# Performance work log

Measured on AMD Instinct MI355X. Metric: run time of the kernel, lower is better.

Reference implementation:

```python
import jax, jax.numpy as jnp
import numpy as np

B, S, D, H = 4, 4096, 512, 8


def setup_inputs() -> dict:
    key = jax.random.key(0)
    ks = jax.random.split(key, 9)
    s = 1.0 / np.sqrt(D)
    return {
        "x": jax.random.normal(ks[0], (B, S, D), jnp.float32),
        "Wq": jax.random.normal(ks[1], (D, D), jnp.float32) * s,
        "bq": jax.random.normal(ks[2], (D,), jnp.float32) * 0.02,
        "Wk": jax.random.normal(ks[3], (D, D), jnp.float32) * s,
        "bk": jax.random.normal(ks[4], (D,), jnp.float32) * 0.02,
        "Wv": jax.random.normal(ks[5], (D, D), jnp.float32) * s,
        "bv": jax.random.normal(ks[6], (D,), jnp.float32) * 0.02,
        "Wo": jax.random.normal(ks[7], (H * D, D), jnp.float32) * (1.0 / np.sqrt(H * D)),
        "bo": jax.random.normal(ks[8], (D,), jnp.float32) * 0.02,
        "num_heads": H,
    }


def reference(x, Wq, bq, Wk, bk, Wv, bv, Wo, bo, num_heads):
    # Q/K/V projections (self-attention path; encoder_output=None)
    q = x @ Wq + bq  # [B,S,D]
    k = x @ Wk + bk
    v = x @ Wv + bv
    scale = 1.0 / jnp.sqrt(jnp.asarray(x.shape[-1], x.dtype))
    scores = jnp.einsum("bqd,bkd->bqk", q, k) * scale  # [B,S,S]
    probs = jax.nn.softmax(scores, axis=-1)
    attn = jnp.einsum("bqk,bkd->bqd", probs, v)  # [B,S,D]
    # Original stacks identical heads then torch.cat along dim=-1 -> tile H copies.
    cat = jnp.tile(attn, (1, 1, num_heads))  # [B,S,H*D]
    return cat @ Wo + bo  # [B,S,D]
```

## Files before the change

kernel.cpp:

```cpp
#include <hip/hip_runtime.h>
#include <stdint.h>

#define SCALE 0.04419417382415922f

typedef __bf16 bf16x8 __attribute__((ext_vector_type(8)));
typedef float f32x4 __attribute__((ext_vector_type(4)));
typedef uint16_t u16x8 __attribute__((ext_vector_type(8)));

static __device__ __forceinline__ uint16_t f2bf(float f) {
  union { float f; uint32_t u; } v; v.f = f;
  uint32_t u = v.u;
  return (uint16_t)((u + 0x7FFFu + ((u >> 16) & 1u)) >> 16);
}

static __device__ __forceinline__ void gload16(const void* g, void* l) {
  __builtin_amdgcn_global_load_lds(
      (__attribute__((address_space(1))) void*)g,
      (__attribute__((address_space(3))) void*)l, 16, 0, 0);
}

#define P_BAR asm volatile("s_barrier" ::: "memory")
#define P_LGKM do { asm volatile("s_waitcnt lgkmcnt(0)" ::: "memory"); \
                    __builtin_amdgcn_sched_barrier(0); } while (0)


__global__ __launch_bounds__(256)
void convert_x(const float* __restrict__ x, uint16_t* __restrict__ xb) {
  size_t i = ((size_t)blockIdx.x * 256 + threadIdx.x) * 8;
  float4 a = *(const float4*)(x + i);
  float4 b = *(const float4*)(x + i + 4);
  u16x8 o;
  o[0] = f2bf(a.x); o[1] = f2bf(a.y); o[2] = f2bf(a.z); o[3] = f2bf(a.w);
  o[4] = f2bf(b.x); o[5] = f2bf(b.y); o[6] = f2bf(b.z); o[7] = f2bf(b.w);
  *(u16x8*)(xb + i) = o;
}

__global__ __launch_bounds__(256)
void pack_w(const float* __restrict__ Wq, const float* __restrict__ Wk,
            const float* __restrict__ Wv, uint16_t* __restrict__ wt) {
  __shared__ float tile[64][65];
  const int k0 = blockIdx.x * 64, n0 = blockIdx.y * 64, m = blockIdx.z;
  const float* W = (m == 0) ? Wq : ((m == 1) ? Wk : Wv);
  const float scl = (m == 0) ? SCALE : 1.0f;
  const int t = threadIdx.x, r = t >> 2, c0 = (t & 3) * 16;
  #pragma unroll
  for (int j = 0; j < 4; j++) {
    float4 v = *(const float4*)&W[(size_t)(k0 + r) * 512 + n0 + c0 + j * 4];
    tile[r][c0 + j * 4 + 0] = v.x; tile[r][c0 + j * 4 + 1] = v.y;
    tile[r][c0 + j * 4 + 2] = v.z; tile[r][c0 + j * 4 + 3] = v.w;
  }
  __syncthreads();
  u16x8 o0, o1;
  #pragma unroll
  for (int e = 0; e < 8; e++) {
    o0[e] = f2bf(tile[c0 + e][r] * scl);
    o1[e] = f2bf(tile[c0 + 8 + e][r] * scl);
  }
  uint16_t* dst = wt + (size_t)(m * 512 + n0 + r) * 512 + k0 + c0;
  *(u16x8*)dst = o0;
  *(u16x8*)(dst + 8) = o1;
}

__global__ __launch_bounds__(256)
void pack_wo(const float* __restrict__ Wo, uint16_t* __restrict__ woT) {
  __shared__ float tile[64][65];
  const int k0 = blockIdx.x * 64, n0 = blockIdx.y * 64;
  const int t = threadIdx.x, r = t >> 2, c0 = (t & 3) * 16;
  float av[16];
  #pragma unroll
  for (int e = 0; e < 16; e++) av[e] = 0.f;
  for (int h = 0; h < 8; h++) {
    const float* src = &Wo[(size_t)(h * 512 + k0 + r) * 512 + n0 + c0];
    #pragma unroll
    for (int j = 0; j < 4; j++) {
      float4 v = *(const float4*)(src + j * 4);
      av[j * 4 + 0] += v.x; av[j * 4 + 1] += v.y;
      av[j * 4 + 2] += v.z; av[j * 4 + 3] += v.w;
    }
  }
  #pragma unroll
  for (int e = 0; e < 16; e++) tile[r][c0 + e] = av[e];
  __syncthreads();
  u16x8 o0, o1;
  #pragma unroll
  for (int e = 0; e < 8; e++) {
    o0[e] = f2bf(tile[c0 + e][r]);
    o1[e] = f2bf(tile[c0 + 8 + e][r]);
  }
  uint16_t* dst = woT + (size_t)(n0 + r) * 512 + k0 + c0;
  *(u16x8*)dst = o0;
  *(u16x8*)(dst + 8) = o1;
}

__global__ void pack_bias(const float* __restrict__ bq, const float* __restrict__ bk,
                          const float* __restrict__ bv, float* __restrict__ bqkv) {
  int i = blockIdx.x * 256 + threadIdx.x;
  if (i < 512) bqkv[i] = bq[i] * SCALE;
  else if (i < 1024) bqkv[i] = bk[i - 512];
  else if (i < 1536) bqkv[i] = bv[i - 1024];
}

__global__ __launch_bounds__(256)
void transpose_v(const uint16_t* __restrict__ qkv, uint16_t* __restrict__ Vt) {
  __shared__ uint16_t tile[64][72];
  const int s0 = blockIdx.x * 64, d0 = blockIdx.y * 64, b = blockIdx.z;
  const int t = threadIdx.x, r = t >> 2, c0 = (t & 3) * 16;
  const uint16_t* src = qkv + ((size_t)(b * 4096 + s0 + r)) * 1536 + 1024 + d0 + c0;
  *(u16x8*)&tile[r][c0] = *(const u16x8*)src;
  *(u16x8*)&tile[r][c0 + 8] = *(const u16x8*)(src + 8);
  __syncthreads();
  u16x8 o0, o1;
  #pragma unroll
  for (int e = 0; e < 8; e++) { o0[e] = tile[c0 + e][r]; o1[e] = tile[c0 + 8 + e][r]; }
  uint16_t* dst = Vt + ((size_t)b * 512 + d0 + r) * 4096 + s0 + c0;
  *(u16x8*)dst = o0;
  *(u16x8*)(dst + 8) = o1;
}

template<int BN, int MODE>
__global__ __launch_bounds__(512, 2)
void gemm8(const uint16_t* __restrict__ A, const uint16_t* __restrict__ Bt,
           const float* __restrict__ bias, void* __restrict__ Cout,
           float* __restrict__ sums,
           int M, int N, int K, int lda, int ldb, int ldc,
           long long aZ, long long bZ, long long cZ, long long sZ) {
  constexpr int NREP = BN / 64;
  constexpr int NH = NREP / 2;
  constexpr int WN = BN / 4;
  constexpr int BELTS = BN * 64;
  __shared__ uint16_t SH[32768 + 2 * BELTS];

  const int nbn = N / BN;
  const int nwg = (M >> 8) * nbn;
  int id = blockIdx.x;
  id = (id & 7) * (nwg >> 3) + (id >> 3);
  const int bm = id / nbn, bn = id % nbn;
  const long long z = blockIdx.z;
  A += z * aZ; Bt += z * bZ;
  const size_t m0 = (size_t)bm * 256, n0 = (size_t)bn * BN;

  const int t = threadIdx.x;
  const int lane = t & 63, w = t >> 6;
  const int wr = w >> 2, wc = w & 3;
  const int l15 = lane & 15, l4 = lane >> 4, l7 = lane & 7, l3 = lane >> 3;
  const int sw = l7 ^ l3;

  const uint16_t* srcA = A + (m0 + w * 8 + l3) * (size_t)lda + sw * 8;
  const uint16_t* srcB = (BN == 256)
      ? Bt + (n0 + (w >> 1) * 64 + (w & 1) * 16 + l3) * (size_t)ldb + sw * 8
      : Bt + (n0 + (w >> 1) * 32 + (w & 1) * 8 + l3) * (size_t)ldb + sw * 8;

  const int NKT = K >> 6;
  const int NIT = NKT >> 1;

  f32x4 acc[8][NREP];
  #pragma unroll
  for (int i = 0; i < 8; i++)
    #pragma unroll
    for (int j = 0; j < NREP; j++) acc[i][j] = (f32x4)(0.f);

  bf16x8 a[4][2], b0[NH][2], b1[NH][2];

  auto stageA = [&](int tile, int mh) {
    const uint16_t* s = srcA + mh * 64 * (size_t)lda + tile * 64;
    uint16_t* d = SH + (tile & 1) * 16384 + mh * 4096 + w * 512;
    gload16(s, d);
    gload16(s + 128 * (size_t)lda, d + 8192);
  };
  auto stageB = [&](int tile, int nh) {
    if (BN == 256) {
      const uint16_t* s = srcB + nh * 32 * (size_t)ldb + tile * 64;
      uint16_t* d = SH + 32768 + (tile & 1) * BELTS + (w >> 1) * 4096 + nh * 2048 + (w & 1) * 1024;
      gload16(s, d);
      gload16(s + 8 * (size_t)ldb, d + 512);
    } else {
      const uint16_t* s = srcB + nh * 16 * (size_t)ldb + tile * 64;
      uint16_t* d = SH + 32768 + (tile & 1) * BELTS + (w >> 1) * 2048 + nh * 1024 + (w & 1) * 512;
      gload16(s, d);
    }
  };
  auto loadA = [&](int buf, int mh) {
    const uint16_t* base = SH + buf * 16384 + (wr * 128 + mh * 64 + l15) * 64;
    #pragma unroll
    for (int m = 0; m < 4; m++)
      #pragma unroll
      for (int ks = 0; ks < 2; ks++)
        a[m][ks] = *(const bf16x8*)(base + m * 1024 + (((ks * 4 + l4) ^ l7) * 8));
  };
  auto loadB = [&](int buf, int nh, bf16x8 (&bd)[NH][2]) {
    const uint16_t* base = SH + 32768 + buf * BELTS + (wc * WN + nh * (WN / 2) + l15) * 64;
    #pragma unroll
    for (int n = 0; n < NH; n++)
      #pragma unroll
      for (int ks = 0; ks < 2; ks++)
        bd[n][ks] = *(const bf16x8*)(base + n * 1024 + (((ks * 4 + l4) ^ l7) * 8));
  };
  auto quad = [&](int mh, int nq, bf16x8 (&bq)[NH][2]) {
    __builtin_amdgcn_s_setprio(1);
    #pragma unroll
    for (int m = 0; m < 4; m++)
      #pragma unroll
      for (int n = 0; n < NH; n++)
        #pragma unroll
        for (int ks = 0; ks < 2; ks++)
          acc[mh * 4 + m][nq + n] = __builtin_amdgcn_mfma_f32_16x16x32_bf16(
              a[m][ks], bq[n][ks], acc[mh * 4 + m][nq + n], 0, 0, 0);
    __builtin_amdgcn_s_setprio(0);
  };

  stageA(0, 0); stageB(0, 0); stageA(0, 1); stageB(0, 1);
  stageA(1, 0); stageB(1, 0); stageA(1, 1);
  if (BN == 256) asm volatile("s_waitcnt vmcnt(6)" ::: "memory");
  else           asm volatile("s_waitcnt vmcnt(5)" ::: "memory");
  P_BAR;

  for (int k = 0; k < NIT - 1; ++k) {
    const int tt = 2 * k;
    loadA(0, 0); loadB(0, 0, b0); stageB(tt + 1, 1);
    P_BAR; P_LGKM; quad(0, 0, b0); P_BAR;
    loadB(0, 1, b1); stageA(tt + 2, 0);
    P_BAR; P_LGKM; quad(0, NH, b1); P_BAR;
    loadA(0, 1); stageB(tt + 2, 0);
    P_BAR; P_LGKM; quad(1, NH, b1); P_BAR;
    stageA(tt + 2, 1);
    if (BN == 256) asm volatile("s_waitcnt vmcnt(6)" ::: "memory");
    else           asm volatile("s_waitcnt vmcnt(5)" ::: "memory");
    P_BAR; quad(1, 0, b0); P_BAR;
    loadA(1, 0); loadB(1, 0, b0); stageB(tt + 2, 1);
    P_BAR; P_LGKM; quad(0, 0, b0); P_BAR;
    loadB(1, 1, b1); stageA(tt + 3, 0);
    P_BAR; P_LGKM; quad(0, NH, b1); P_BAR;
    loadA(1, 1); stageB(tt + 3, 0);
    P_BAR; P_LGKM; quad(1, NH, b1); P_BAR;
    stageA(tt + 3, 1);
    if (BN == 256) asm volatile("s_waitcnt vmcnt(6)" ::: "memory");
    else           asm volatile("s_waitcnt vmcnt(5)" ::: "memory");
    P_BAR; quad(1, 0, b0); P_BAR;
  }
  loadA(0, 0); loadB(0, 0, b0); stageB(NKT - 1, 1);
  P_BAR; P_LGKM; quad(0, 0, b0); P_BAR;
  loadB(0, 1, b1);
  P_BAR; P_LGKM; quad(0, NH, b1); P_BAR;
  loadA(0, 1);
  P_BAR; P_LGKM; quad(1, NH, b1); P_BAR;
  asm volatile("s_waitcnt vmcnt(0)" ::: "memory");
  P_BAR; quad(1, 0, b0); P_BAR;
  loadA(1, 0); loadB(1, 0, b0);
  P_BAR; P_LGKM; quad(0, 0, b0); P_BAR;
  loadB(1, 1, b1);
  P_BAR; P_LGKM; quad(0, NH, b1); P_BAR;
  loadA(1, 1);
  P_BAR; P_LGKM; quad(1, NH, b1); P_BAR;
  quad(1, 0, b0);

  asm volatile("s_waitcnt vmcnt(0) lgkmcnt(0)" ::: "memory");
  __syncthreads();

  const int g = l4;

  if (MODE == 1) {
    float bvv[NREP];
    #pragma unroll
    for (int ni = 0; ni < NREP; ni++) bvv[ni] = bias[n0 + wc * WN + ni * 16 + l15];
    float* C = (float*)Cout + z * cZ;
    #pragma unroll
    for (int am = 0; am < 8; am++)
      #pragma unroll
      for (int r = 0; r < 4; r++) {
        size_t gr = m0 + wr * 128 + am * 16 + g * 4 + r;
        #pragma unroll
        for (int ni = 0; ni < NREP; ni++)
          C[gr * (size_t)ldc + n0 + wc * WN + ni * 16 + l15] = acc[am][ni][r] + bvv[ni];
      }
    return;
  }

  if (MODE == 2) {
    #pragma unroll
    for (int am = 0; am < 8; am++)
      #pragma unroll
      for (int r = 0; r < 4; r++) {
        float s = 0.f;
        #pragma unroll
        for (int ni = 0; ni < NREP; ni++) {
          float v = __expf(acc[am][ni][r]);
          acc[am][ni][r] = v;
          s += v;
        }
        s += __shfl_xor(s, 1); s += __shfl_xor(s, 2);
        s += __shfl_xor(s, 4); s += __shfl_xor(s, 8);
        if (l15 == 0)
          sums[z * sZ + (m0 + wr * 128 + am * 16 + g * 4 + r) * 64 + (n0 >> 6) + wc] = s;
      }
  }

  float bvv[NREP];
  #pragma unroll
  for (int ni = 0; ni < NREP; ni++)
    bvv[ni] = (MODE == 0) ? bias[n0 + wc * WN + ni * 16 + l15] : 0.f;
  float4 sc[8];
  if (MODE == 3) {
    #pragma unroll
    for (int am = 0; am < 8; am++)
      sc[am] = *(const float4*)&sums[z * sZ + m0 + wr * 128 + am * 16 + g * 4];
  }

  constexpr int STR = BN + 8;
  uint16_t* C16 = (uint16_t*)Cout + z * cZ;
  #pragma unroll
  for (int h = 0; h < 2; ++h) {
    __syncthreads();
    if (wr == h) {
      #pragma unroll
      for (int am = 0; am < 8; am++)
        #pragma unroll
        for (int r = 0; r < 4; r++) {
          const int lr = am * 16 + g * 4 + r;
          #pragma unroll
          for (int ni = 0; ni < NREP; ni++) {
            float v = acc[am][ni][r] + bvv[ni];
            if (MODE == 3) v *= ((const float*)&sc[am])[r];
            SH[lr * STR + wc * WN + ni * 16 + l15] = f2bf(v);
          }
        }
    }
    __syncthreads();
    constexpr int CPT = BN / 32;
    #pragma unroll
    for (int c = 0; c < CPT; ++c) {
      const int idx = t + c * 512;
      const int row = idx / (BN / 8), c8 = idx % (BN / 8);
      *(u16x8*)(C16 + (m0 + h * 128 + row) * (size_t)ldc + n0 + c8 * 8) =
          *(const u16x8*)(SH + row * STR + c8 * 8);
    }
  }
}

__global__ __launch_bounds__(256)
void reduce_sums(const float* __restrict__ P, float* __restrict__ inv, int rows) {
  int r = blockIdx.x * 256 + threadIdx.x;
  if (r >= rows) return;
  const float4* p4 = (const float4*)(P + (size_t)r * 64);
  float s = 0.f;
  #pragma unroll
  for (int i = 0; i < 16; ++i) { float4 v = p4[i]; s += (v.x + v.y) + (v.z + v.w); }
  inv[r] = 1.f / s;
}


extern "C" void kernel_launch(void* const* d_in, const int* in_sizes, int n_in,
                              void* d_out, int out_size, void* d_ws, size_t ws_size,
                              hipStream_t stream) {
  const float* x   = (const float*)d_in[0];
  const float* Wq  = (const float*)d_in[1];
  const float* bq  = (const float*)d_in[2];
  const float* Wk  = (const float*)d_in[3];
  const float* bk  = (const float*)d_in[4];
  const float* Wv  = (const float*)d_in[5];
  const float* bvp = (const float*)d_in[6];
  const float* Wo  = (const float*)d_in[7];
  const float* bo  = (const float*)d_in[8];
  float* out = (float*)d_out;

  char* ws = (char*)d_ws;
  const size_t MB = (size_t)1 << 20;
  uint16_t* qkv   = (uint16_t*)(ws);
  uint16_t* Vt    = (uint16_t*)(ws + 48 * MB);
  uint16_t* attn  = (uint16_t*)(ws + 64 * MB);
  uint16_t* wqkvT = (uint16_t*)(ws + 80 * MB);
  uint16_t* woT   = (uint16_t*)(ws + 82 * MB);
  float*    bqkv  = (float*)   (ws + 83 * MB);
  float*    sumsP = (float*)   (ws + 84 * MB);
  float*    invs  = (float*)   (ws + 88 * MB);
  uint16_t* Sbuf  = (uint16_t*)(ws + 96 * MB);
  uint16_t* xb    = (uint16_t*)(ws + 96 * MB);

  const int nz = (ws_size >= 225 * MB) ? 4 : 2;

  convert_x<<<dim3(4096), dim3(256), 0, stream>>>(x, xb);
  pack_w<<<dim3(8, 8, 3), dim3(256), 0, stream>>>(Wq, Wk, Wv, wqkvT);
  pack_wo<<<dim3(8, 8), dim3(256), 0, stream>>>(Wo, woT);
  pack_bias<<<dim3(6), dim3(256), 0, stream>>>(bq, bk, bvp, bqkv);

  gemm8<256, 0><<<dim3(384, 1, 1), dim3(512), 0, stream>>>(
      xb, wqkvT, bqkv, qkv, nullptr,
      16384, 1536, 512, 512, 512, 1536, 0, 0, 0, 0);

  transpose_v<<<dim3(64, 8, 4), dim3(256), 0, stream>>>(qkv, Vt);

  for (int p = 0; p < 4 / nz; ++p) {
    const uint16_t* qb = qkv + (size_t)p * nz * 4096 * 1536;
    float* sp = sumsP + (size_t)p * nz * 4096 * 64;
    float* ip = invs + (size_t)p * nz * 4096;
    gemm8<256, 2><<<dim3(256, 1, nz), dim3(512), 0, stream>>>(
        qb, qb + 512, nullptr, Sbuf, sp,
        4096, 4096, 512, 1536, 1536, 4096,
        (long long)4096 * 1536, (long long)4096 * 1536, (long long)4096 * 4096,
        (long long)4096 * 64);
    reduce_sums<<<dim3(nz * 4096 / 256), dim3(256), 0, stream>>>(sp, ip, nz * 4096);
    gemm8<128, 3><<<dim3(64, 1, nz), dim3(512), 0, stream>>>(
        Sbuf, Vt + (size_t)p * nz * 512 * 4096, nullptr,
        attn + (size_t)p * nz * 4096 * 512, ip,
        4096, 512, 4096, 4096, 4096, 512,
        (long long)4096 * 4096, (long long)512 * 4096, (long long)4096 * 512,
        4096);
  }

  gemm8<128, 1><<<dim3(256, 1, 1), dim3(512), 0, stream>>>(
      attn, woT, bo, out, nullptr,
      16384, 512, 512, 512, 512, 512, 0, 0, 0, 0);
}
```

Baseline: 272.1 us.

## Fold Wq·Wkᵀ into one matrix and compute scores against raw x

Rewrites the scores as x·(Wq·Wkᵀ)·xᵀ plus a per-key bias vector. A small 512x512 GEMM builds the combined weight, one GEMM produces Y=x·W2 together with V, and a new strip-scheduled scores kernel multiplies Y by bf16 x directly with the exp and partial-sum epilogue inlined. This drops the separate K projection and shrinks the projection output width from 1536 to 1024. In exchange it adds several small setup kernels (bias folding, a c-vector pass) and rounds the combined weight to bf16, which changes numerical error. Query-dependent bias terms are dropped because softmax cancels them.

```diff
diff --git a/kernel.cpp b/kernel.cpp
--- a/kernel.cpp
+++ b/kernel.cpp
@@ -11,6 +11,10 @@
   union { float f; uint32_t u; } v; v.f = f;
   uint32_t u = v.u;
   return (uint16_t)((u + 0x7FFFu + ((u >> 16) & 1u)) >> 16);
+}
+static __device__ __forceinline__ float bf2f(uint16_t h) {
+  union { uint32_t u; float f; } v; v.u = ((uint32_t)h) << 16;
+  return v.f;
 }
 
 static __device__ __forceinline__ void gload16(const void* g, void* l) {
@@ -36,16 +40,30 @@
 }
 
 __global__ __launch_bounds__(256)
-void pack_w(const float* __restrict__ Wq, const float* __restrict__ Wk,
-            const float* __restrict__ Wv, uint16_t* __restrict__ wt) {
+void pack_wraw(const float* __restrict__ Wq, const float* __restrict__ Wk,
+               uint16_t* __restrict__ oq, uint16_t* __restrict__ ok) {
+  size_t i = ((size_t)blockIdx.x * 256 + threadIdx.x) * 8;
+  const float* src = blockIdx.y ? Wk : Wq;
+  uint16_t* dst = blockIdx.y ? ok : oq;
+  const float scl = blockIdx.y ? 1.0f : SCALE;
+  float4 a = *(const float4*)(src + i);
+  float4 b = *(const float4*)(src + i + 4);
+  u16x8 o;
+  o[0] = f2bf(a.x * scl); o[1] = f2bf(a.y * scl);
+  o[2] = f2bf(a.z * scl); o[3] = f2bf(a.w * scl);
+  o[4] = f2bf(b.x * scl); o[5] = f2bf(b.y * scl);
+  o[6] = f2bf(b.z * scl); o[7] = f2bf(b.w * scl);
+  *(u16x8*)(dst + i) = o;
+}
+
+__global__ __launch_bounds__(256)
+void pack_wv(const float* __restrict__ Wv, uint16_t* __restrict__ wvT) {
   __shared__ float tile[64][65];
-  const int k0 = blockIdx.x * 64, n0 = blockIdx.y * 64, m = blockIdx.z;
-  const float* W = (m == 0) ? Wq : ((m == 1) ? Wk : Wv);
-  const float scl = (m == 0) ? SCALE : 1.0f;
+  const int k0 = blockIdx.x * 64, n0 = blockIdx.y * 64;
   const int t = threadIdx.x, r = t >> 2, c0 = (t & 3) * 16;
   #pragma unroll
   for (int j = 0; j < 4; j++) {
-    float4 v = *(const float4*)&W[(size_t)(k0 + r) * 512 + n0 + c0 + j * 4];
+    float4 v = *(const float4*)&Wv[(size_t)(k0 + r) * 512 + n0 + c0 + j * 4];
     tile[r][c0 + j * 4 + 0] = v.x; tile[r][c0 + j * 4 + 1] = v.y;
     tile[r][c0 + j * 4 + 2] = v.z; tile[r][c0 + j * 4 + 3] = v.w;
   }
@@ -53,10 +71,10 @@
   u16x8 o0, o1;
   #pragma unroll
   for (int e = 0; e < 8; e++) {
-    o0[e] = f2bf(tile[c0 + e][r] * scl);
-    o1[e] = f2bf(tile[c0 + 8 + e][r] * scl);
-  }
-  uint16_t* dst = wt + (size_t)(m * 512 + n0 + r) * 512 + k0 + c0;
+    o0[e] = f2bf(tile[c0 + e][r]);
+    o1[e] = f2bf(tile[c0 + 8 + e][r]);
+  }
+  uint16_t* dst = wvT + (size_t)(n0 + r) * 512 + k0 + c0;
   *(u16x8*)dst = o0;
   *(u16x8*)(dst + 8) = o1;
 }
@@ -92,20 +110,56 @@
   *(u16x8*)(dst + 8) = o1;
 }
 
-__global__ void pack_bias(const float* __restrict__ bq, const float* __restrict__ bk,
-                          const float* __restrict__ bv, float* __restrict__ bqkv) {
+__global__ void pack_byv(const float* __restrict__ bv, float* __restrict__ byv) {
   int i = blockIdx.x * 256 + threadIdx.x;
-  if (i < 512) bqkv[i] = bq[i] * SCALE;
-  else if (i < 1024) bqkv[i] = bk[i - 512];
-  else if (i < 1536) bqkv[i] = bv[i - 1024];
+  if (i < 512) byv[i] = 0.f;
+  else if (i < 1024) byv[i] = bv[i - 512];
+}
+
+__global__ __launch_bounds__(512)
+void pack_gc(const float* __restrict__ Wk, const float* __restrict__ bq,
+             const float* __restrict__ bk, float* __restrict__ g) {
+  __shared__ float red[512];
+  const int m = threadIdx.x;
+  float s = 0.f;
+  for (int d = 0; d < 512; ++d) s += Wk[(size_t)m * 512 + d] * bq[d];
+  g[m] = s * SCALE;
+  red[m] = bk[m] * bq[m];
+  __syncthreads();
+  for (int o = 256; o; o >>= 1) {
+    if (m < o) red[m] += red[m + o];
+    __syncthreads();
+  }
+  if (m == 0) g[512] = red[0] * SCALE;
 }
 
 __global__ __launch_bounds__(256)
-void transpose_v(const uint16_t* __restrict__ qkv, uint16_t* __restrict__ Vt) {
+void c_vec(const uint16_t* __restrict__ xb, const float* __restrict__ g,
+           float* __restrict__ cv) {
+  __shared__ float gs[513];
+  const int t = threadIdx.x;
+  for (int i = t; i < 513; i += 256) gs[i] = g[i];
+  __syncthreads();
+  const int r = blockIdx.x * 32 + (t >> 3);
+  const int j = t & 7;
+  const uint16_t* p = xb + (size_t)r * 512 + j * 64;
+  float s = 0.f;
+  #pragma unroll
+  for (int q = 0; q < 8; q++) {
+    u16x8 v = *(const u16x8*)(p + q * 8);
+    #pragma unroll
+    for (int e = 0; e < 8; e++) s += bf2f(v[e]) * gs[j * 64 + q * 8 + e];
+  }
+  s += __shfl_xor(s, 1); s += __shfl_xor(s, 2); s += __shfl_xor(s, 4);
+  if (j == 0) cv[r] = s + gs[512];
+}
+
+__global__ __launch_bounds__(256)
+void transpose_v(const uint16_t* __restrict__ yv, uint16_t* __restrict__ Vt) {
   __shared__ uint16_t tile[64][72];
   const int s0 = blockIdx.x * 64, d0 = blockIdx.y * 64, b = blockIdx.z;
   const int t = threadIdx.x, r = t >> 2, c0 = (t & 3) * 16;
-  const uint16_t* src = qkv + ((size_t)(b * 4096 + s0 + r)) * 1536 + 1024 + d0 + c0;
+  const uint16_t* src = yv + ((size_t)(b * 4096 + s0 + r)) * 1024 + 512 + d0 + c0;
   *(u16x8*)&tile[r][c0] = *(const u16x8*)src;
   *(u16x8*)&tile[r][c0 + 8] = *(const u16x8*)(src + 8);
   __syncthreads();
@@ -118,12 +172,12 @@
 }
 
 template<int BN, int MODE>
-__global__ __launch_bounds__(512, 2)
-void gemm8(const uint16_t* __restrict__ A, const uint16_t* __restrict__ Bt,
-           const float* __restrict__ bias, void* __restrict__ Cout,
-           float* __restrict__ sums,
-           int M, int N, int K, int lda, int ldb, int ldc,
-           long long aZ, long long bZ, long long cZ, long long sZ) {
+static __device__ __forceinline__
+void gemm8_body(const uint16_t* __restrict__ A, const uint16_t* __restrict__ Bt,
+                const float* __restrict__ bias, void* __restrict__ Cout,
+                const float* __restrict__ sums,
+                int M, int N, int K, int lda, int ldb, int ldc,
+                long long aZ, long long bZ, long long cZ, long long sZ) {
   constexpr int NREP = BN / 64;
   constexpr int NH = NREP / 2;
   constexpr int WN = BN / 4;
@@ -275,29 +329,10 @@
     return;
   }
 
-  if (MODE == 2) {
-    #pragma unroll
-    for (int am = 0; am < 8; am++)
-      #pragma unroll
-      for (int r = 0; r < 4; r++) {
-        float s = 0.f;
-        #pragma unroll
-        for (int ni = 0; ni < NREP; ni++) {
-          float v = __expf(acc[am][ni][r]);
-          acc[am][ni][r] = v;
-          s += v;
-        }
-        s += __shfl_xor(s, 1); s += __shfl_xor(s, 2);
-        s += __shfl_xor(s, 4); s += __shfl_xor(s, 8);
-        if (l15 == 0)
-          sums[z * sZ + (m0 + wr * 128 + am * 16 + g * 4 + r) * 64 + (n0 >> 6) + wc] = s;
-      }
-  }
-
   float bvv[NREP];
   #pragma unroll
   for (int ni = 0; ni < NREP; ni++)
-    bvv[ni] = (MODE == 0) ? bias[n0 + wc * WN + ni * 16 + l15] : 0.f;
+    bvv[ni] = (MODE == 0 && bias) ? bias[n0 + wc * WN + ni * 16 + l15] : 0.f;
   float4 sc[8];
   if (MODE == 3) {
     #pragma unroll
@@ -336,6 +371,197 @@
   }
 }
 
+__global__ __launch_bounds__(512, 2)
+void w2_gemm(const uint16_t* A, const uint16_t* Bt, void* C) {
+  gemm8_body<128, 0>(A, Bt, nullptr, C, nullptr, 512, 512, 512, 512, 512, 512, 0, 0, 0, 0);
+}
+__global__ __launch_bounds__(512, 2)
+void yv_gemm(const uint16_t* A, const uint16_t* Bt, const float* bias, void* C) {
+  gemm8_body<256, 0>(A, Bt, bias, C, nullptr, 16384, 1024, 512, 512, 512, 1024, 0, 0, 0, 0);
+}
+__global__ __launch_bounds__(512, 2)
+void pv_gemm(const uint16_t* A, const uint16_t* Bt, void* C, const float* inv) {
+  gemm8_body<128, 3>(A, Bt, nullptr, C, inv, 4096, 512, 4096, 4096, 4096, 512,
+                     (long long)4096 * 4096, (long long)512 * 4096,
+                     (long long)4096 * 512, 4096);
+}
+__global__ __launch_bounds__(512, 2)
+void out_gemm(const uint16_t* A, const uint16_t* Bt, const float* bias, void* C) {
+  gemm8_body<128, 1>(A, Bt, bias, C, nullptr, 16384, 512, 512, 512, 512, 512, 0, 0, 0, 0);
+}
+
+__global__ __launch_bounds__(512, 2)
+void scores_strip(const uint16_t* __restrict__ Y, const uint16_t* __restrict__ X,
+                  const float* __restrict__ cvec, uint16_t* __restrict__ Sout,
+                  float* __restrict__ sums) {
+  __shared__ uint16_t SH[65536];
+  int id = blockIdx.x;
+  id = (id & 7) * 8 + (id >> 3);
+  const int bm = id >> 2, sc = id & 3;
+  const long long z = blockIdx.z;
+  const size_t m0 = (size_t)bm * 256;
+  const int t = threadIdx.x, lane = t & 63, w = t >> 6;
+  const int wr = w >> 2, wc = w & 3;
+  const int l15 = lane & 15, l4 = lane >> 4, l7 = lane & 7, l3 = lane >> 3;
+  const int sw = l7 ^ l3;
+
+  const uint16_t* Yz = Y + z * (4096ll * 1024);
+  const uint16_t* Xz = X + z * (4096ll * 512);
+  const uint16_t* srcA = Yz + (m0 + w * 8 + l3) * 1024 + sw * 8;
+  const uint16_t* srcB0 = Xz + ((w >> 1) * 64 + (w & 1) * 16 + l3) * 512 + sw * 8;
+  const uint16_t* srcB;
+
+  bf16x8 a[4][2], b0[2][2], b1[2][2];
+  f32x4 acc[8][4];
+
+  auto stageA = [&](int tile, int mh) {
+    const uint16_t* s = srcA + mh * 64 * 1024 + tile * 64;
+    uint16_t* d = SH + (tile & 1) * 16384 + mh * 4096 + w * 512;
+    gload16(s, d);
+    gload16(s + 128 * 1024, d + 8192);
+  };
+  auto stageB = [&](int tile, int nh) {
+    const uint16_t* s = srcB + nh * 32 * 512 + tile * 64;
+    uint16_t* d = SH + 32768 + (tile & 1) * 16384 + (w >> 1) * 4096 + nh * 2048 + (w & 1) * 1024;
+    gload16(s, d);
+    gload16(s + 8 * 512, d + 512);
+  };
+  auto loadA = [&](int buf, int mh) {
+    const uint16_t* base = SH + buf * 16384 + (wr * 128 + mh * 64 + l15) * 64;
+    #pragma unroll
+    for (int m = 0; m < 4; m++)
+      #pragma unroll
+      for (int ks = 0; ks < 2; ks++)
+        a[m][ks] = *(const bf16x8*)(base + m * 1024 + (((ks * 4 + l4) ^ l7) * 8));
+  };
+  auto loadB = [&](int buf, int nh, bf16x8 (&bd)[2][2]) {
+    const uint16_t* base = SH + 32768 + buf * 16384 + (wc * 64 + nh * 32 + l15) * 64;
+    #pragma unroll
+    for (int n = 0; n < 2; n++)
+      #pragma unroll
+      for (int ks = 0; ks < 2; ks++)
+        bd[n][ks] = *(const bf16x8*)(base + n * 1024 + (((ks * 4 + l4) ^ l7) * 8));
+  };
+  auto quad = [&](int mh, int nq, bf16x8 (&bq)[2][2]) {
+    __builtin_amdgcn_s_setprio(1);
+    #pragma unroll
+    for (int m = 0; m < 4; m++)
+      #pragma unroll
+      for (int n = 0; n < 2; n++)
+        #pragma unroll
+        for (int ks = 0; ks < 2; ks++)
+          acc[mh * 4 + m][nq + n] = __builtin_amdgcn_mfma_f32_16x16x32_bf16(
+              a[m][ks], bq[n][ks], acc[mh * 4 + m][nq + n], 0, 0, 0);
+    __builtin_amdgcn_s_setprio(0);
+  };
+
+  #pragma unroll 1
+  for (int js = 0; js < 4; ++js) {
+    const size_t n0 = (size_t)sc * 1024 + (size_t)js * 256;
+    srcB = srcB0 + n0 * 512;
+    #pragma unroll
+    for (int i = 0; i < 8; i++)
+      #pragma unroll
+      for (int j = 0; j < 4; j++) acc[i][j] = (f32x4)(0.f);
+
+    __syncthreads();
+
+    stageA(0, 0); stageB(0, 0); stageA(0, 1); stageB(0, 1);
+    stageA(1, 0); stageB(1, 0); stageA(1, 1);
+    asm volatile("s_waitcnt vmcnt(6)" ::: "memory");
+    P_BAR;
+
+    #pragma unroll 1
+    for (int k = 0; k < 3; ++k) {
+      const int tt = 2 * k;
+      loadA(0, 0); loadB(0, 0, b0); stageB(tt + 1, 1);
+      P_BAR; P_LGKM; quad(0, 0, b0); P_BAR;
+      loadB(0, 1, b1); stageA(tt + 2, 0);
+      P_BAR; P_LGKM; quad(0, 2, b1); P_BAR;
+      loadA(0, 1); stageB(tt + 2, 0);
+      P_BAR; P_LGKM; quad(1, 2, b1); P_BAR;
+      stageA(tt + 2, 1);
+      asm volatile("s_waitcnt vmcnt(6)" ::: "memory");
+      P_BAR; quad(1, 0, b0); P_BAR;
+      loadA(1, 0); loadB(1, 0, b0); stageB(tt + 2, 1);
+      P_BAR; P_LGKM; quad(0, 0, b0); P_BAR;
+      loadB(1, 1, b1); stageA(tt + 3, 0);
+      P_BAR; P_LGKM; quad(0, 2, b1); P_BAR;
+      loadA(1, 1); stageB(tt + 3, 0);
+      P_BAR; P_LGKM; quad(1, 2, b1); P_BAR;
+      stageA(tt + 3, 1);
+      asm volatile("s_waitcnt vmcnt(6)" ::: "memory");
+      P_BAR; quad(1, 0, b0); P_BAR;
+    }
+    loadA(0, 0); loadB(0, 0, b0); stageB(7, 1);
+    P_BAR; P_LGKM; quad(0, 0, b0); P_BAR;
+    loadB(0, 1, b1);
+    P_BAR; P_LGKM; quad(0, 2, b1); P_BAR;
+    loadA(0, 1);
+    P_BAR; P_LGKM; quad(1, 2, b1); P_BAR;
+    asm volatile("s_waitcnt vmcnt(0)" ::: "memory");
+    P_BAR; quad(1, 0, b0); P_BAR;
+    loadA(1, 0); loadB(1, 0, b0);
+    P_BAR; P_LGKM; quad(0, 0, b0); P_BAR;
+    loadB(1, 1, b1);
+    P_BAR; P_LGKM; quad(0, 2, b1); P_BAR;
+    loadA(1, 1);
+    P_BAR; P_LGKM; quad(1, 2, b1); P_BAR;
+    quad(1, 0, b0);
+
+    asm volatile("s_waitcnt vmcnt(0) lgkmcnt(0)" ::: "memory");
+    __syncthreads();
+
+    const int g = l4;
+    const float* cz = cvec + z * 4096 + n0;
+    float cvv[4];
+    #pragma unroll
+    for (int ni = 0; ni < 4; ni++) cvv[ni] = cz[wc * 64 + ni * 16 + l15];
+    #pragma unroll
+    for (int am = 0; am < 8; am++)
+      #pragma unroll
+      for (int r = 0; r < 4; r++) {
+        float s = 0.f;
+        #pragma unroll
+        for (int ni = 0; ni < 4; ni++) {
+          float v = __expf(acc[am][ni][r] + cvv[ni]);
+          acc[am][ni][r] = v;
+          s += v;
+        }
+        s += __shfl_xor(s, 1); s += __shfl_xor(s, 2);
+        s += __shfl_xor(s, 4); s += __shfl_xor(s, 8);
+        if (l15 == 0)
+          sums[z * (4096ll * 64) + (m0 + wr * 128 + am * 16 + g * 4 + r) * 64 +
+               sc * 16 + js * 4 + wc] = s;
+      }
+
+    uint16_t* C16 = Sout + z * (4096ll * 4096);
+    #pragma unroll
+    for (int h = 0; h < 2; ++h) {
+      __syncthreads();
+      if (wr == h) {
+        #pragma unroll
+        for (int am = 0; am < 8; am++)
+          #pragma unroll
+          for (int r = 0; r < 4; r++) {
+            const int lr = am * 16 + g * 4 + r;
+            #pragma unroll
+            for (int ni = 0; ni < 4; ni++)
+              SH[lr * 264 + wc * 64 + ni * 16 + l15] = f2bf(acc[am][ni][r]);
+          }
+      }
+      __syncthreads();
+      #pragma unroll
+      for (int c = 0; c < 8; ++c) {
+        const int idx = t + c * 512;
+        const int row = idx >> 5, c8 = idx & 31;
+        *(u16x8*)(C16 + (m0 + h * 128 + row) * 4096 + n0 + c8 * 8) =
+            *(const u16x8*)(SH + row * 264 + c8 * 8);
+      }
+    }
+  }
+}
+
 __global__ __launch_bounds__(256)
 void reduce_sums(const float* __restrict__ P, float* __restrict__ inv, int rows) {
   int r = blockIdx.x * 256 + threadIdx.x;
@@ -364,49 +590,49 @@
 
   char* ws = (char*)d_ws;
   const size_t MB = (size_t)1 << 20;
-  uint16_t* qkv   = (uint16_t*)(ws);
-  uint16_t* Vt    = (uint16_t*)(ws + 48 * MB);
-  uint16_t* attn  = (uint16_t*)(ws + 64 * MB);
-  uint16_t* wqkvT = (uint16_t*)(ws + 80 * MB);
-  uint16_t* woT   = (uint16_t*)(ws + 82 * MB);
-  float*    bqkv  = (float*)   (ws + 83 * MB);
-  float*    sumsP = (float*)   (ws + 84 * MB);
-  float*    invs  = (float*)   (ws + 88 * MB);
-  uint16_t* Sbuf  = (uint16_t*)(ws + 96 * MB);
-  uint16_t* xb    = (uint16_t*)(ws + 96 * MB);
+  uint16_t* xb   = (uint16_t*)(ws);
+  uint16_t* yv   = (uint16_t*)(ws + 16 * MB);
+  uint16_t* Vt   = (uint16_t*)(ws + 48 * MB);
+  uint16_t* attn = (uint16_t*)(ws + 64 * MB);
+  uint16_t* wqs  = (uint16_t*)(ws + 80 * MB);
+  uint16_t* wkr  = (uint16_t*)(ws + 80 * MB + 512 * 1024);
+  uint16_t* w2T  = (uint16_t*)(ws + 81 * MB);
+  uint16_t* wvT  = (uint16_t*)(ws + 81 * MB + 512 * 1024);
+  uint16_t* woT  = (uint16_t*)(ws + 82 * MB);
+  float*    byv  = (float*)   (ws + 82 * MB + 512 * 1024);
+  float*    g    = (float*)   (ws + 83 * MB);
+  float*    sums = (float*)   (ws + 84 * MB);
+  float*    invs = (float*)   (ws + 88 * MB);
+  float*    cv   = (float*)   (ws + 89 * MB);
+  uint16_t* Sbuf = (uint16_t*)(ws + 96 * MB);
 
   const int nz = (ws_size >= 225 * MB) ? 4 : 2;
 
   convert_x<<<dim3(4096), dim3(256), 0, stream>>>(x, xb);
-  pack_w<<<dim3(8, 8, 3), dim3(256), 0, stream>>>(Wq, Wk, Wv, wqkvT);
+  pack_wraw<<<dim3(128, 2), dim3(256), 0, stream>>>(Wq, Wk, wqs, wkr);
+  pack_wv<<<dim3(8, 8), dim3(256), 0, stream>>>(Wv, wvT);
   pack_wo<<<dim3(8, 8), dim3(256), 0, stream>>>(Wo, woT);
-  pack_bias<<<dim3(6), dim3(256), 0, stream>>>(bq, bk, bvp, bqkv);
-
-  gemm8<256, 0><<<dim3(384, 1, 1), dim3(512), 0, stream>>>(
-      xb, wqkvT, bqkv, qkv, nullptr,
-      16384, 1536, 512, 512, 512, 1536, 0, 0, 0, 0);
-
-  transpose_v<<<dim3(64, 8, 4), dim3(256), 0, stream>>>(qkv, Vt);
+  pack_byv<<<dim3(4), dim3(256), 0, stream>>>(bvp, byv);
+  pack_gc<<<dim3(1), dim3(512), 0, stream>>>(Wk, bq, bk, g);
+
+  w2_gemm<<<dim3(8, 1, 1), dim3(512), 0, stream>>>(wkr, wqs, w2T);
+
+  yv_gemm<<<dim3(256, 1, 1), dim3(512), 0, stream>>>(xb, w2T, byv, yv);
+
+  transpose_v<<<dim3(64, 8, 4), dim3(256), 0, stream>>>(yv, Vt);
+  c_vec<<<dim3(512), dim3(256), 0, stream>>>(xb, g, cv);
 
   for (int p = 0; p < 4 / nz; ++p) {
-    const uint16_t* qb = qkv + (size_t)p * nz * 4096 * 1536;
-    float* sp = sumsP + (size_t)p * nz * 4096 * 64;
+    const uint16_t* Yp = yv + (size_t)p * nz * 4096 * 1024;
+    const uint16_t* Xp = xb + (size_t)p * nz * 4096 * 512;
+    const float* cp = cv + (size_t)p * nz * 4096;
+    float* sp = sums + (size_t)p * nz * 4096 * 64;
     float* ip = invs + (size_t)p * nz * 4096;
-    gemm8<256, 2><<<dim3(256, 1, nz), dim3(512), 0, stream>>>(
-        qb, qb + 512, nullptr, Sbuf, sp,
-        4096, 4096, 512, 1536, 1536, 4096,
-        (long long)4096 * 1536, (long long)4096 * 1536, (long long)4096 * 4096,
-        (long long)4096 * 64);
+    scores_strip<<<dim3(64, 1, nz), dim3(512), 0, stream>>>(Yp, Xp, cp, Sbuf, sp);
     reduce_sums<<<dim3(nz * 4096 / 256), dim3(256), 0, stream>>>(sp, ip, nz * 4096);
-    gemm8<128, 3><<<dim3(64, 1, nz), dim3(512), 0, stream>>>(
-        Sbuf, Vt + (size_t)p * nz * 512 * 4096, nullptr,
-        attn + (size_t)p * nz * 4096 * 512, ip,
-        4096, 512, 4096, 4096, 4096, 512,
-        (long long)4096 * 4096, (long long)512 * 4096, (long long)4096 * 512,
-        4096);
-  }
-
-  gemm8<128, 1><<<dim3(256, 1, 1), dim3(512), 0, stream>>>(
-      attn, woT, bo, out, nullptr,
-      16384, 512, 512, 512, 512, 512, 0, 0, 0, 0);
-}
+    pv_gemm<<<dim3(64, 1, nz), dim3(512), 0, stream>>>(
+        Sbuf, Vt + (size_t)p * nz * 512 * 4096, attn + (size_t)p * nz * 4096 * 512, ip);
+  }
+
+  out_gemm<<<dim3(256, 1, 1), dim3(512), 0, stream>>>(attn, woT, bo, out);
+}
```

Measured after the change: 404.5 us. 1.49x slower.
